# Optimization experiments

Hardware: AMD Instinct MI355X
Metric: run time of the kernel (lower is better)

Reference implementation:

```python
import jax, jax.numpy as jnp
import numpy as np

RES = 100          # resolution
ITERS = 1000       # lowfid solver iterations
INIT_MIN = 0.01    # conductivity floor (init_min)
BATCH = 32
HIDDEN = [128, 256, 512]


def conductivity_original(pores, res):
    """Coarse 5x5 pore map -> base conductivity on the fine res x res grid.
    pore present (1) -> low conductivity (0), solid (0) -> conductivity 1."""
    B = pores.shape[0]
    grid = 1.0 - pores.reshape(B, 5, 5)
    f = res // 5
    return jnp.repeat(jnp.repeat(grid, f, axis=1), f, axis=2)  # (B, res, res)


def mlp_forward(x, params):
    n = len(params)
    for i, (W, b) in enumerate(params):
        x = x @ W + b
        if i < n - 1:
            x = jax.nn.relu(x)
    return x


def lowfid_solve(k):
    """1000-iteration Jacobi relaxation of variable-coefficient steady heat
    equation with T=1 on top edge, T=0 on bottom edge, insulated sides.
    Returns effective conductivity kappa per sample, shape (B,)."""
    B, res, _ = k.shape
    # face conductivities (arithmetic mean of adjacent cells, edge-padded)
    kp = jnp.pad(k, ((0, 0), (1, 1), (1, 1)), mode='edge')
    kN = 0.5 * (k + kp[:, :-2, 1:-1])
    kS = 0.5 * (k + kp[:, 2:, 1:-1])
    kW = 0.5 * (k + kp[:, 1:-1, :-2])
    kE = 0.5 * (k + kp[:, 1:-1, 2:])
    denom = kN + kS + kW + kE + 1e-12

    def step(T, _):
        Tp = jnp.pad(T, ((0, 0), (0, 0), (1, 1)), mode='edge')        # side Neumann
        Tp = jnp.pad(Tp, ((0, 0), (1, 1), (0, 0)))                    # top/bottom Dirichlet
        Tp = Tp.at[:, 0, :].set(1.0)                                   # T=1 at top, T=0 at bottom
        T_new = (kN * Tp[:, :-2, 1:-1] + kS * Tp[:, 2:, 1:-1]
                 + kW * Tp[:, 1:-1, :-2] + kE * Tp[:, 1:-1, 2:]) / denom
        return T_new, None

    T0 = jnp.broadcast_to(jnp.linspace(1.0, 0.0, res)[None, :, None], (B, res, res))
    T, _ = jax.lax.scan(step, T0, None, length=ITERS)
    # heat flux through top boundary; domain size 1, dT = 1 -> kappa = mean flux
    kappa = jnp.mean(2.0 * res * k[:, 0, :] * (1.0 - T[:, 0, :]), axis=1)
    return kappa


def setup_inputs() -> dict:
    key = jax.random.key(0)
    ks = jax.random.split(key, 10)
    pores = (jax.random.uniform(ks[0], (BATCH, 25)) > 0.5).astype(jnp.float32)
    sizes = [25] + HIDDEN + [RES * RES]
    inp = {"pores": pores}
    for i in range(len(sizes) - 1):
        fan_in = sizes[i]
        W = jax.random.normal(ks[1 + 2 * i], (sizes[i], sizes[i + 1]), jnp.float32) * np.sqrt(2.0 / fan_in)
        b = jnp.zeros((sizes[i + 1],), jnp.float32)
        inp[f"W{i + 1}"] = W
        inp[f"b{i + 1}"] = b
    return inp


def reference(pores, W1, b1, W2, b2, W3, b3, W4, b4):
    params = [(W1, b1), (W2, b2), (W3, b3), (W4, b4)]
    B = pores.shape[0]
    gen = mlp_forward(pores.reshape(B, 25), params).reshape(B, RES, RES)
    cond = gen + conductivity_original(pores, RES)   # learn_residual
    cond = jnp.maximum(cond, INIT_MIN)               # relu clamp to init_min
    kappa = lowfid_solve(cond)
    return kappa, cond
```

## Files before the change

kernel.cpp:

```cpp
#include <hip/hip_runtime.h>
#include <hip/hip_bf16.h>

#define RES   100
#define ITERS 1000
#define SLOTP 128

typedef float vf2 __attribute__((ext_vector_type(2)));

__global__ __launch_bounds__(256) void mlp123(const float* __restrict__ pores,
                                              const float* __restrict__ W1, const float* __restrict__ b1,
                                              const float* __restrict__ W2, const float* __restrict__ b2,
                                              const float* __restrict__ W3, const float* __restrict__ b3,
                                              float* __restrict__ x3out) {
    __shared__ float x1[128];
    __shared__ float x2[256];
    const int s = blockIdx.x, tid = threadIdx.x;

    if (tid < 128) {
        float acc = b1[tid];
#pragma unroll
        for (int k = 0; k < 25; ++k)
            acc = fmaf(pores[s * 25 + k], W1[k * 128 + tid], acc);
        x1[tid] = fmaxf(acc, 0.0f);
    }
    __syncthreads();

    {
        float acc = b2[tid];
#pragma unroll 8
        for (int k = 0; k < 128; ++k)
            acc = fmaf(x1[k], W2[k * 256 + tid], acc);
        x2[tid] = fmaxf(acc, 0.0f);
    }
    __syncthreads();

    {
        float a0 = b3[tid], a1 = b3[tid + 256];
#pragma unroll 8
        for (int k = 0; k < 256; ++k) {
            float xv = x2[k];
            a0 = fmaf(xv, W3[k * 512 + tid],       a0);
            a1 = fmaf(xv, W3[k * 512 + tid + 256], a1);
        }
        x3out[s * 512 + tid]       = fmaxf(a0, 0.0f);
        x3out[s * 512 + tid + 256] = fmaxf(a1, 0.0f);
    }
}

__global__ __launch_bounds__(256) void fc4_fused(const float* __restrict__ X3,
                                                 const float* __restrict__ W4,
                                                 const float* __restrict__ b4,
                                                 const float* __restrict__ pores,
                                                 float* __restrict__ cond) {
    const int j = blockIdx.x * 256 + threadIdx.x;
    if (j >= RES * RES) return;
    const int bg = blockIdx.y;
    const float* x = X3 + bg * 8 * 512;

    float acc[8];
    float bj = b4[j];
#pragma unroll
    for (int b = 0; b < 8; ++b) acc[b] = bj;

    for (int k0 = 0; k0 < 512; k0 += 8) {
        float w[8];
#pragma unroll
        for (int u = 0; u < 8; ++u)
            w[u] = W4[(k0 + u) * (RES * RES) + j];
#pragma unroll
        for (int u = 0; u < 8; ++u) {
#pragma unroll
            for (int b = 0; b < 8; ++b)
                acc[b] = fmaf(x[b * 512 + k0 + u], w[u], acc[b]);
        }
    }

    const int row = j / RES, col = j % RES;
    const int p = (row / 20) * 5 + (col / 20);
#pragma unroll
    for (int b = 0; b < 8; ++b) {
        int bb = bg * 8 + b;
        float base = 1.0f - pores[bb * 25 + p];
        cond[bb * RES * RES + j] = fmaxf(acc[b] + base, 0.01f);
    }
}

__device__ __forceinline__ float dpp_shr1(float old_v, float src) {
    return __int_as_float(__builtin_amdgcn_update_dpp(
        __float_as_int(old_v), __float_as_int(src), 0x138, 0xf, 0xf, false));
}
__device__ __forceinline__ float dpp_shl1(float old_v, float src) {
    return __int_as_float(__builtin_amdgcn_update_dpp(
        __float_as_int(old_v), __float_as_int(src), 0x130, 0xf, 0xf, false));
}

template<int R>
__device__ __forceinline__ void jstep(const vf2* __restrict__ nptr, const vf2* __restrict__ sptr,
                                      vf2* __restrict__ topptr, vf2* __restrict__ botptr,
                                      const vf2* wN, const vf2* wS,
                                      const vf2* wA, const vf2* wB,
                                      const vf2* Tin, vf2* Tout, bool fix49) {
    vf2 nval = *nptr;
    vf2 sval = *sptr;
#pragma unroll
    for (int r = 0; r < R; ++r) {
        vf2 nb = (r == 0)     ? nval : Tin[r - 1];
        vf2 sb = (r == R - 1) ? sval : Tin[r + 1];
        float lo = Tin[r].x, hi = Tin[r].y;
        float wlo = dpp_shr1(lo, hi);
        float ehi = dpp_shl1(hi, lo);
        ehi = fix49 ? hi : ehi;
        vf2 P1; P1.x = wlo; P1.y = ehi;
        vf2 TS; TS.x = hi;  TS.y = lo;
        Tout[r] = wN[r] * nb + wS[r] * sb + wA[r] * P1 + wB[r] * TS;
    }
    *topptr = Tout[0];
    *botptr = Tout[R - 1];
}

__global__ __launch_bounds__(1024) void jacobi(const float* __restrict__ cond,
                                               float* __restrict__ kappa_out) {
    __shared__ float kst[RES * RES];
    __shared__ float SA[34 * SLOTP];
    __shared__ float SB[34 * SLOTP];

    const int b   = blockIdx.x;
    const int tid = threadIdx.x;

    for (int i = tid; i < RES * RES; i += 1024)
        kst[i] = cond[b * RES * RES + i];
    if (tid < SLOTP) {
        SA[32 * SLOTP + tid] = 1.0f;  SA[33 * SLOTP + tid] = 0.0f;
        SB[32 * SLOTP + tid] = 1.0f;  SB[33 * SLOTP + tid] = 0.0f;
    }
    __syncthreads();

    const int w    = tid >> 6;
    const int lane = tid & 63;
    const int R    = (w < 4) ? 7 : 6;
    const int r0   = (w < 4) ? 7 * w : 28 + 6 * (w - 4);
    const int c0   = min(2 * lane, 98), c1 = c0 + 1;
    const int lane2 = 2 * lane;
    const bool fix49 = (lane == 49);

    vf2 wN[7], wS[7], wA[7], wB[7], T0[7], T1[7];

#pragma unroll
    for (int r = 0; r < 7; ++r) {
        if (r < R) {
            int i   = r0 + r;
            int in_ = i ? i - 1 : 0;
            int is_ = (i < RES - 1) ? i + 1 : RES - 1;
            int jw  = c0 ? c0 - 1 : 0;
            int je  = (c1 < RES - 1) ? c1 + 1 : RES - 1;
            float kc0 = kst[i * RES + c0], kc1 = kst[i * RES + c1];
            float kn0 = 0.5f * (kc0 + kst[in_ * RES + c0]);
            float kn1 = 0.5f * (kc1 + kst[in_ * RES + c1]);
            float ks0 = 0.5f * (kc0 + kst[is_ * RES + c0]);
            float ks1 = 0.5f * (kc1 + kst[is_ * RES + c1]);
            float kw0 = 0.5f * (kc0 + kst[i * RES + jw]);
            float kw1 = 0.5f * (kc1 + kc0);
            float ke0 = 0.5f * (kc0 + kc1);
            float ke1 = 0.5f * (kc1 + kst[i * RES + je]);
            float inv0 = 1.0f / (kn0 + ks0 + kw0 + ke0 + 1e-12f);
            float inv1 = 1.0f / (kn1 + ks1 + kw1 + ke1 + 1e-12f);
            wN[r].x = kn0 * inv0;  wN[r].y = kn1 * inv1;
            wS[r].x = ks0 * inv0;  wS[r].y = ks1 * inv1;
            wA[r].x = kw0 * inv0;  wA[r].y = ke1 * inv1;
            wB[r].x = ke0 * inv0;  wB[r].y = kw1 * inv1;
            float v = 1.0f - (float)i * (1.0f / (RES - 1));
            T0[r].x = v;  T0[r].y = v;
        }
    }

    vf2 bot0 = (w < 4) ? T0[6] : T0[5];
    *(vf2*)(SA + (2 * w) * SLOTP + lane2)     = T0[0];
    *(vf2*)(SA + (2 * w + 1) * SLOTP + lane2) = bot0;
    __syncthreads();

    const int nslot = (w == 0)  ? 32 : (2 * w - 1);
    const int sslot = (w == 15) ? 33 : (2 * w + 2);
    const int topsl = 2 * w;

    const vf2* SAn = (const vf2*)(SA + nslot * SLOTP + lane2);
    const vf2* SAs = (const vf2*)(SA + sslot * SLOTP + lane2);
    const vf2* SBn = (const vf2*)(SB + nslot * SLOTP + lane2);
    const vf2* SBs = (const vf2*)(SB + sslot * SLOTP + lane2);
    vf2* SAtop = (vf2*)(SA + topsl * SLOTP + lane2);
    vf2* SAbot = (vf2*)(SA + (topsl + 1) * SLOTP + lane2);
    vf2* SBtop = (vf2*)(SB + topsl * SLOTP + lane2);
    vf2* SBbot = (vf2*)(SB + (topsl + 1) * SLOTP + lane2);

    for (int it = 0; it < ITERS / 2; ++it) {
        if (w < 4) jstep<7>(SAn, SAs, SBtop, SBbot, wN, wS, wA, wB, T0, T1, fix49);
        else       jstep<6>(SAn, SAs, SBtop, SBbot, wN, wS, wA, wB, T0, T1, fix49);
        __syncthreads();
        if (w < 4) jstep<7>(SBn, SBs, SAtop, SAbot, wN, wS, wA, wB, T1, T0, fix49);
        else       jstep<6>(SBn, SBs, SAtop, SAbot, wN, wS, wA, wB, T1, T0, fix49);
        __syncthreads();
    }

    if (w == 0) {
        float s = 0.0f;
        if (lane < 50)
            s = kst[c0] * (1.0f - T0[0].x) + kst[c1] * (1.0f - T0[0].y);
        for (int off = 32; off; off >>= 1)
            s += __shfl_down(s, off);
        if (lane == 0) kappa_out[b] = 2.0f * s;
    }
}

extern "C" void kernel_launch(void* const* d_in, const int* in_sizes, int n_in,
                              void* d_out, int out_size, void* d_ws, size_t ws_size,
                              hipStream_t stream) {
    (void)in_sizes; (void)n_in; (void)out_size; (void)ws_size;
    const float* pores = (const float*)d_in[0];
    const float* W1 = (const float*)d_in[1];
    const float* b1 = (const float*)d_in[2];
    const float* W2 = (const float*)d_in[3];
    const float* b2 = (const float*)d_in[4];
    const float* W3 = (const float*)d_in[5];
    const float* b3 = (const float*)d_in[6];
    const float* W4 = (const float*)d_in[7];
    const float* b4 = (const float*)d_in[8];

    float* x3 = (float*)d_ws;

    float* kappa = (float*)d_out;
    float* cond  = kappa + 32;

    mlp123<<<32, 256, 0, stream>>>(pores, W1, b1, W2, b2, W3, b3, x3);
    fc4_fused<<<dim3(40, 4), 256, 0, stream>>>(x3, W4, b4, pores, cond);
    jacobi<<<32, 1024, 0, stream>>>(cond, kappa);
}
```

Before: 647.0 us.

## Use two-row halos to run two Jacobi sweeps per barrier

The Jacobi kernel now exchanges two-row halos through shared memory, so each wave recomputes one ghost row on each side and advances two iterations between barriers. This halves the number of __syncthreads calls and LDS exchanges, at the cost of redundant ghost-row arithmetic and more registers for the extra weight rows. It also drops the shared-memory copy of the conductivity field and reads the coefficients straight from global memory during setup.

```diff
diff --git a/kernel.cpp b/kernel.cpp
--- a/kernel.cpp
+++ b/kernel.cpp
@@ -85,6 +85,7 @@
     }
 }
 
+
 __device__ __forceinline__ float dpp_shr1(float old_v, float src) {
     return __int_as_float(__builtin_amdgcn_update_dpp(
         __float_as_int(old_v), __float_as_int(src), 0x138, 0xf, 0xf, false));
@@ -94,116 +95,140 @@
         __float_as_int(old_v), __float_as_int(src), 0x130, 0xf, 0xf, false));
 }
 
-template<int R>
-__device__ __forceinline__ void jstep(const vf2* __restrict__ nptr, const vf2* __restrict__ sptr,
-                                      vf2* __restrict__ topptr, vf2* __restrict__ botptr,
-                                      const vf2* wN, const vf2* wS,
-                                      const vf2* wA, const vf2* wB,
-                                      const vf2* Tin, vf2* Tout, bool fix49) {
-    vf2 nval = *nptr;
-    vf2 sval = *sptr;
-#pragma unroll
-    for (int r = 0; r < R; ++r) {
-        vf2 nb = (r == 0)     ? nval : Tin[r - 1];
-        vf2 sb = (r == R - 1) ? sval : Tin[r + 1];
-        float lo = Tin[r].x, hi = Tin[r].y;
-        float wlo = dpp_shr1(lo, hi);
-        float ehi = dpp_shl1(hi, lo);
-        ehi = fix49 ? hi : ehi;
-        vf2 P1; P1.x = wlo; P1.y = ehi;
-        vf2 TS; TS.x = hi;  TS.y = lo;
-        Tout[r] = wN[r] * nb + wS[r] * sb + wA[r] * P1 + wB[r] * TS;
-    }
-    *topptr = Tout[0];
-    *botptr = Tout[R - 1];
+__device__ __forceinline__ vf2 rowstep(vf2 n, vf2 c, vf2 s,
+                                       vf2 wn, vf2 ws, vf2 ww, vf2 we, bool fix49) {
+    float lo = c.x, hi = c.y;
+    float wlo = dpp_shr1(lo, hi);
+    float e   = dpp_shl1(hi, lo);
+    float ehi = fix49 ? hi : e;
+    vf2 r;
+    r.x = fmaf(wn.x, n.x, fmaf(ws.x, s.x, fmaf(ww.x, wlo, we.x * hi)));
+    r.y = fmaf(wn.y, n.y, fmaf(ws.y, s.y, fmaf(we.y, ehi, ww.y * lo)));
+    return r;
+}
+
+template<int R, bool TOP, bool BOT>
+__device__ __forceinline__ void superstep(const float* __restrict__ srcN,
+                                          const float* __restrict__ srcS,
+                                          float* __restrict__ dst,
+                                          const vf2* wN, const vf2* wS,
+                                          const vf2* wW, const vf2* wE,
+                                          vf2* T, bool fix49) {
+    vf2 hN2, hN1, hS0, hS1;
+    if (!TOP) {
+        hN2 = *(const vf2*)(srcN);
+        hN1 = *(const vf2*)(srcN + SLOTP);
+    } else { hN1.x = 1.0f; hN1.y = 1.0f; hN2 = hN1; }
+    if (!BOT) {
+        hS0 = *(const vf2*)(srcS);
+        hS1 = *(const vf2*)(srcS + SLOTP);
+    } else { hS0.x = 0.0f; hS0.y = 0.0f; hS1 = hS0; }
+
+    vf2 U[R + 2];
+    if (TOP) { U[0].x = 1.0f; U[0].y = 1.0f; }
+    else     U[0] = rowstep(hN2, hN1, T[0], wN[0], wS[0], wW[0], wE[0], fix49);
+    U[1] = rowstep(hN1, T[0], T[1], wN[1], wS[1], wW[1], wE[1], fix49);
+#pragma unroll
+    for (int i = 2; i <= R - 1; ++i)
+        U[i] = rowstep(T[i - 2], T[i - 1], T[i], wN[i], wS[i], wW[i], wE[i], fix49);
+    U[R] = rowstep(T[R - 2], T[R - 1], hS0, wN[R], wS[R], wW[R], wE[R], fix49);
+    if (BOT) { U[R + 1].x = 0.0f; U[R + 1].y = 0.0f; }
+    else     U[R + 1] = rowstep(T[R - 1], hS0, hS1, wN[R + 1], wS[R + 1], wW[R + 1], wE[R + 1], fix49);
+
+#pragma unroll
+    for (int j = 0; j < R; ++j)
+        T[j] = rowstep(U[j], U[j + 1], U[j + 2], wN[j + 1], wS[j + 1], wW[j + 1], wE[j + 1], fix49);
+
+    *(vf2*)(dst)             = T[0];
+    *(vf2*)(dst + SLOTP)     = T[1];
+    *(vf2*)(dst + 2 * SLOTP) = T[R - 2];
+    *(vf2*)(dst + 3 * SLOTP) = T[R - 1];
 }
 
 __global__ __launch_bounds__(1024) void jacobi(const float* __restrict__ cond,
                                                float* __restrict__ kappa_out) {
-    __shared__ float kst[RES * RES];
-    __shared__ float SA[34 * SLOTP];
-    __shared__ float SB[34 * SLOTP];
+    __shared__ float SA[64 * SLOTP];
+    __shared__ float SB[64 * SLOTP];
 
     const int b   = blockIdx.x;
     const int tid = threadIdx.x;
-
-    for (int i = tid; i < RES * RES; i += 1024)
-        kst[i] = cond[b * RES * RES + i];
-    if (tid < SLOTP) {
-        SA[32 * SLOTP + tid] = 1.0f;  SA[33 * SLOTP + tid] = 0.0f;
-        SB[32 * SLOTP + tid] = 1.0f;  SB[33 * SLOTP + tid] = 0.0f;
-    }
-    __syncthreads();
+    const float* condp = cond + b * RES * RES;
 
     const int w    = tid >> 6;
     const int lane = tid & 63;
     const int R    = (w < 4) ? 7 : 6;
-    const int r0   = (w < 4) ? 7 * w : 28 + 6 * (w - 4);
+    const int a    = (w < 4) ? 7 * w : 28 + 6 * (w - 4);
     const int c0   = min(2 * lane, 98), c1 = c0 + 1;
     const int lane2 = 2 * lane;
     const bool fix49 = (lane == 49);
 
-    vf2 wN[7], wS[7], wA[7], wB[7], T0[7], T1[7];
-
-#pragma unroll
-    for (int r = 0; r < 7; ++r) {
-        if (r < R) {
-            int i   = r0 + r;
-            int in_ = i ? i - 1 : 0;
-            int is_ = (i < RES - 1) ? i + 1 : RES - 1;
+    vf2 wN[9], wS[9], wW[9], wE[9], T[7];
+
+#pragma unroll
+    for (int i = 0; i < 9; ++i) {
+        int row = a - 1 + i;
+        if (i < R + 2 && row >= 0 && row < RES) {
+            int in_ = row ? row - 1 : 0;
+            int is_ = (row < RES - 1) ? row + 1 : RES - 1;
             int jw  = c0 ? c0 - 1 : 0;
             int je  = (c1 < RES - 1) ? c1 + 1 : RES - 1;
-            float kc0 = kst[i * RES + c0], kc1 = kst[i * RES + c1];
-            float kn0 = 0.5f * (kc0 + kst[in_ * RES + c0]);
-            float kn1 = 0.5f * (kc1 + kst[in_ * RES + c1]);
-            float ks0 = 0.5f * (kc0 + kst[is_ * RES + c0]);
-            float ks1 = 0.5f * (kc1 + kst[is_ * RES + c1]);
-            float kw0 = 0.5f * (kc0 + kst[i * RES + jw]);
+            float kc0 = condp[row * RES + c0], kc1 = condp[row * RES + c1];
+            float kn0 = 0.5f * (kc0 + condp[in_ * RES + c0]);
+            float kn1 = 0.5f * (kc1 + condp[in_ * RES + c1]);
+            float ks0 = 0.5f * (kc0 + condp[is_ * RES + c0]);
+            float ks1 = 0.5f * (kc1 + condp[is_ * RES + c1]);
+            float kw0 = 0.5f * (kc0 + condp[row * RES + jw]);
             float kw1 = 0.5f * (kc1 + kc0);
             float ke0 = 0.5f * (kc0 + kc1);
-            float ke1 = 0.5f * (kc1 + kst[i * RES + je]);
+            float ke1 = 0.5f * (kc1 + condp[row * RES + je]);
             float inv0 = 1.0f / (kn0 + ks0 + kw0 + ke0 + 1e-12f);
             float inv1 = 1.0f / (kn1 + ks1 + kw1 + ke1 + 1e-12f);
-            wN[r].x = kn0 * inv0;  wN[r].y = kn1 * inv1;
-            wS[r].x = ks0 * inv0;  wS[r].y = ks1 * inv1;
-            wA[r].x = kw0 * inv0;  wA[r].y = ke1 * inv1;
-            wB[r].x = ke0 * inv0;  wB[r].y = kw1 * inv1;
-            float v = 1.0f - (float)i * (1.0f / (RES - 1));
-            T0[r].x = v;  T0[r].y = v;
-        }
-    }
-
-    vf2 bot0 = (w < 4) ? T0[6] : T0[5];
-    *(vf2*)(SA + (2 * w) * SLOTP + lane2)     = T0[0];
-    *(vf2*)(SA + (2 * w + 1) * SLOTP + lane2) = bot0;
+            wN[i].x = kn0 * inv0;  wN[i].y = kn1 * inv1;
+            wS[i].x = ks0 * inv0;  wS[i].y = ks1 * inv1;
+            wW[i].x = kw0 * inv0;  wW[i].y = kw1 * inv1;
+            wE[i].x = ke0 * inv0;  wE[i].y = ke1 * inv1;
+        }
+    }
+
+#pragma unroll
+    for (int j = 0; j < 7; ++j)
+        if (j < R) {
+            float v = 1.0f - (float)(a + j) * (1.0f / (RES - 1));
+            T[j].x = v;  T[j].y = v;
+        }
+
+    const int nb = (w > 0)  ? (4 * w - 2) : 0;
+    const int sb = (w < 15) ? (4 * w + 4) : 60;
+    const float* SAn = SA + lane2 + nb * SLOTP;
+    const float* SAs = SA + lane2 + sb * SLOTP;
+    float*       SAd = SA + lane2 + (4 * w) * SLOTP;
+    const float* SBn = SB + lane2 + nb * SLOTP;
+    const float* SBs = SB + lane2 + sb * SLOTP;
+    float*       SBd = SB + lane2 + (4 * w) * SLOTP;
+
+    *(vf2*)(SAd)             = T[0];
+    *(vf2*)(SAd + SLOTP)     = T[1];
+    *(vf2*)(SAd + 2 * SLOTP) = T[R - 2];
+    *(vf2*)(SAd + 3 * SLOTP) = T[R - 1];
     __syncthreads();
 
-    const int nslot = (w == 0)  ? 32 : (2 * w - 1);
-    const int sslot = (w == 15) ? 33 : (2 * w + 2);
-    const int topsl = 2 * w;
-
-    const vf2* SAn = (const vf2*)(SA + nslot * SLOTP + lane2);
-    const vf2* SAs = (const vf2*)(SA + sslot * SLOTP + lane2);
-    const vf2* SBn = (const vf2*)(SB + nslot * SLOTP + lane2);
-    const vf2* SBs = (const vf2*)(SB + sslot * SLOTP + lane2);
-    vf2* SAtop = (vf2*)(SA + topsl * SLOTP + lane2);
-    vf2* SAbot = (vf2*)(SA + (topsl + 1) * SLOTP + lane2);
-    vf2* SBtop = (vf2*)(SB + topsl * SLOTP + lane2);
-    vf2* SBbot = (vf2*)(SB + (topsl + 1) * SLOTP + lane2);
-
-    for (int it = 0; it < ITERS / 2; ++it) {
-        if (w < 4) jstep<7>(SAn, SAs, SBtop, SBbot, wN, wS, wA, wB, T0, T1, fix49);
-        else       jstep<6>(SAn, SAs, SBtop, SBbot, wN, wS, wA, wB, T0, T1, fix49);
+    for (int it = 0; it < ITERS / 4; ++it) {
+        if (w == 0)      superstep<7, true,  false>(SAn, SAs, SBd, wN, wS, wW, wE, T, fix49);
+        else if (w < 4)  superstep<7, false, false>(SAn, SAs, SBd, wN, wS, wW, wE, T, fix49);
+        else if (w < 15) superstep<6, false, false>(SAn, SAs, SBd, wN, wS, wW, wE, T, fix49);
+        else             superstep<6, false, true >(SAn, SAs, SBd, wN, wS, wW, wE, T, fix49);
         __syncthreads();
-        if (w < 4) jstep<7>(SBn, SBs, SAtop, SAbot, wN, wS, wA, wB, T1, T0, fix49);
-        else       jstep<6>(SBn, SBs, SAtop, SAbot, wN, wS, wA, wB, T1, T0, fix49);
+        if (w == 0)      superstep<7, true,  false>(SBn, SBs, SAd, wN, wS, wW, wE, T, fix49);
+        else if (w < 4)  superstep<7, false, false>(SBn, SBs, SAd, wN, wS, wW, wE, T, fix49);
+        else if (w < 15) superstep<6, false, false>(SBn, SBs, SAd, wN, wS, wW, wE, T, fix49);
+        else             superstep<6, false, true >(SBn, SBs, SAd, wN, wS, wW, wE, T, fix49);
         __syncthreads();
     }
 
     if (w == 0) {
         float s = 0.0f;
         if (lane < 50)
-            s = kst[c0] * (1.0f - T0[0].x) + kst[c1] * (1.0f - T0[0].y);
+            s = condp[c0] * (1.0f - T[0].x) + condp[c1] * (1.0f - T[0].y);
         for (int off = 32; off; off >>= 1)
             s += __shfl_down(s, off);
         if (lane == 0) kappa_out[b] = 2.0f * s;
```

Result: slower. 1.125 ms (+73.9%).
